# Optimization experiments

Hardware: AMD Instinct MI355X
Metric: run time of the kernel (lower is better)

## Reference

```python
import jax, jax.numpy as jnp
import numpy as np
from jax import lax

T, B, DIN, DLAT = 512, 512, 64, 128


def setup_inputs() -> dict:
    key = jax.random.key(0)
    ks = jax.random.split(key, 8)
    s = 0.1  # keep gate pre-activations in a sane range
    return {
        "seqs": jax.random.normal(ks[0], (T, B, DIN), dtype=jnp.float32),
        "h": jax.random.normal(ks[1], (B, DLAT), dtype=jnp.float32),
        "Wz": jax.random.normal(ks[2], (DLAT, DIN + DLAT), dtype=jnp.float32) * s,
        "bz": jax.random.normal(ks[3], (DLAT,), dtype=jnp.float32) * s,
        "Wr": jax.random.normal(ks[4], (DLAT, DIN + DLAT), dtype=jnp.float32) * s,
        "br": jax.random.normal(ks[5], (DLAT,), dtype=jnp.float32) * s,
        "Wi": jax.random.normal(ks[6], (DLAT, DIN + DLAT), dtype=jnp.float32) * s,
        "bi": jax.random.normal(ks[7], (DLAT,), dtype=jnp.float32) * s,
    }


def reference(seqs, h, Wz, bz, Wr, br, Wi, bi):
    # seqs: [T, B, DIN], h: [B, DLAT]. Returns all hiddens [T+1, B, DLAT].
    def step(h, x):
        merge = jnp.concatenate([h, x], axis=1)          # [B, DLAT+DIN]
        zt = jax.nn.sigmoid(merge @ Wz.T + bz)           # update gate
        rt = jax.nn.sigmoid(merge @ Wr.T + br)           # reset gate
        cand = jnp.tanh(jnp.concatenate([h * rt, x], axis=1) @ Wi.T + bi)
        h_new = (1.0 - zt) * h + zt * cand
        return h_new, h_new

    _, hs = lax.scan(step, h, seqs)                      # hs: [T, B, DLAT]
    return jnp.concatenate([h[None], hs], axis=0)        # [T+1, B, DLAT]
```

## Files before the change

### kernel.cpp

```cpp
#include <hip/hip_runtime.h>
#include <math.h>

#define TT   512
#define BB   512
#define DIN  64
#define DLAT 128
#define KKK  192
#define NBLK 32
#define TCHUNK 16
#define X_ELEMS ((size_t)TT * BB * 384)
#define X_BYTES (X_ELEMS * 2)

typedef _Float16 half8 __attribute__((ext_vector_type(8)));
typedef _Float16 half4 __attribute__((ext_vector_type(4)));
typedef float    f32x4 __attribute__((ext_vector_type(4)));

#define MFMA16(A, B, C) __builtin_amdgcn_mfma_f32_16x16x32_f16((A), (B), (C), 0, 0, 0)

__device__ __forceinline__ float fsigmoid(float x) {
    float e = __builtin_amdgcn_exp2f(-1.44269504f * x);
    return __builtin_amdgcn_rcpf(1.f + e);
}
__device__ __forceinline__ float ftanh(float x) {
    float e = __builtin_amdgcn_exp2f(2.88539008f * x);
    return 1.f - 2.f * __builtin_amdgcn_rcpf(1.f + e);
}
__device__ __forceinline__ half8 cvt8(float4 a, float4 b) {
    return (half8){(_Float16)a.x, (_Float16)a.y, (_Float16)a.z, (_Float16)a.w,
                   (_Float16)b.x, (_Float16)b.y, (_Float16)b.z, (_Float16)b.w};
}

__global__ __launch_bounds__(256) void xproj(
    const float* __restrict__ seqs,
    const float* __restrict__ Wz, const float* __restrict__ bz,
    const float* __restrict__ Wr, const float* __restrict__ br,
    const float* __restrict__ Wi, const float* __restrict__ bi,
    _Float16* __restrict__ X)
{
    const int tid = threadIdx.x;
    const int w = tid >> 6, l = tid & 63, q = l >> 4, ln = l & 15;
    const int bid = blockIdx.x;
    const int tb  = bid >> 5;
    const int blk = bid & 31;
    const int b0  = blk * 16;

    half8 wzf[2][2], wrf[2][2], wif[2][2];
    float bzv[2], brv[2], biv[2];
    #pragma unroll
    for (int s = 0; s < 2; ++s) {
        const int n = 32 * w + 16 * s + ln;
        #pragma unroll
        for (int kt = 0; kt < 2; ++kt) {
            const int k0 = DLAT + kt * 32 + q * 8;
            wzf[s][kt] = cvt8(*(const float4*)&Wz[n * KKK + k0],
                              *(const float4*)&Wz[n * KKK + k0 + 4]);
            wrf[s][kt] = cvt8(*(const float4*)&Wr[n * KKK + k0],
                              *(const float4*)&Wr[n * KKK + k0 + 4]);
            wif[s][kt] = cvt8(*(const float4*)&Wi[n * KKK + k0],
                              *(const float4*)&Wi[n * KKK + k0 + 4]);
        }
        bzv[s] = bz[n]; brv[s] = br[n]; biv[s] = bi[n];
    }

    for (int tt = 0; tt < TCHUNK; ++tt) {
        const int t = tb * TCHUNK + tt;
        const float* xr = seqs + ((size_t)t * BB + b0 + ln) * DIN + q * 8;
        half8 a0 = cvt8(*(const float4*)xr,        *(const float4*)(xr + 4));
        half8 a1 = cvt8(*(const float4*)(xr + 32), *(const float4*)(xr + 36));

        f32x4 az[2], ar[2], ai[2];
        #pragma unroll
        for (int s = 0; s < 2; ++s) {
            az[s] = (f32x4){bzv[s], bzv[s], bzv[s], bzv[s]};
            ar[s] = (f32x4){brv[s], brv[s], brv[s], brv[s]};
            ai[s] = (f32x4){biv[s], biv[s], biv[s], biv[s]};
        }
        #pragma unroll
        for (int s = 0; s < 2; ++s) {
            az[s] = MFMA16(a0, wzf[s][0], az[s]);
            az[s] = MFMA16(a1, wzf[s][1], az[s]);
            ar[s] = MFMA16(a0, wrf[s][0], ar[s]);
            ar[s] = MFMA16(a1, wrf[s][1], ar[s]);
            ai[s] = MFMA16(a0, wif[s][0], ai[s]);
            ai[s] = MFMA16(a1, wif[s][1], ai[s]);
        }

        half8 o0, o1, o2;
        #pragma unroll
        for (int s = 0; s < 2; ++s)
            #pragma unroll
            for (int i = 0; i < 4; ++i) {
                o0[s * 4 + i] = (_Float16)az[s][i];
                o1[s * 4 + i] = (_Float16)ar[s][i];
                o2[s * 4 + i] = (_Float16)ai[s][i];
            }
        _Float16* xo = X + ((size_t)(t * NBLK + blk) * 256 + tid) * 24;
        *(half8*)xo        = o0;
        *(half8*)(xo +  8) = o1;
        *(half8*)(xo + 16) = o2;
    }
}

__global__ __launch_bounds__(256, 1) void gru_rx(
    const float* __restrict__ h0,
    const float* __restrict__ Wz, const float* __restrict__ Wr,
    const float* __restrict__ Wi,
    const _Float16* __restrict__ X, float* __restrict__ out)
{
    __shared__ __align__(16) _Float16 hA [16][136];
    __shared__ __align__(16) _Float16 hrA[16][136];

    const int tid = threadIdx.x;
    const int w = tid >> 6, l = tid & 63, q = l >> 4, ln = l & 15;
    const int blk = (int)blockIdx.x;
    const int b0  = blk * 16;

    half8 wzf[2][4], wrf[2][4], wif[2][4];
    #pragma unroll
    for (int s = 0; s < 2; ++s) {
        const int n = 32 * w + 16 * s + ln;
        #pragma unroll
        for (int kt = 0; kt < 4; ++kt) {
            const int k0 = kt * 32 + q * 8;
            wzf[s][kt] = cvt8(*(const float4*)&Wz[n * KKK + k0],
                              *(const float4*)&Wz[n * KKK + k0 + 4]);
            wrf[s][kt] = cvt8(*(const float4*)&Wr[n * KKK + k0],
                              *(const float4*)&Wr[n * KKK + k0 + 4]);
            wif[s][kt] = cvt8(*(const float4*)&Wi[n * KKK + k0],
                              *(const float4*)&Wi[n * KKK + k0 + 4]);
        }
    }

    float h[2][4];
    #pragma unroll
    for (int s = 0; s < 2; ++s)
        #pragma unroll
        for (int i = 0; i < 4; ++i)
            h[s][i] = h0[(size_t)(b0 + 4 * q + i) * DLAT + 32 * w + 16 * s + ln];

    for (int idx = tid; idx < 16 * DLAT; idx += 256) {
        const int m = idx >> 7, c = idx & 127;
        const float v = h0[(size_t)(b0 + m) * DLAT + c];
        out[(size_t)(b0 + m) * DLAT + c] = v;
        hA[m][c] = (_Float16)v;
    }

    half8 xc0, xc1, xc2;
    {
        const _Float16* xp = X + ((size_t)(0 * NBLK + blk) * 256 + tid) * 24;
        xc0 = *(const half8*)xp;
        xc1 = *(const half8*)(xp + 8);
        xc2 = *(const half8*)(xp + 16);
    }
    __syncthreads();

    for (int t = 0; t < TT; ++t) {
        half8 xn0, xn1, xn2;
        const bool have = (t + 1 < TT);
        if (have) {
            const _Float16* xp = X + ((size_t)((t + 1) * NBLK + blk) * 256 + tid) * 24;
            xn0 = *(const half8*)xp;
            xn1 = *(const half8*)(xp + 8);
            xn2 = *(const half8*)(xp + 16);
        }

        half8 a0 = *(const half8*)&hA[ln][ 0 + q * 8];
        half8 a1 = *(const half8*)&hA[ln][32 + q * 8];
        half8 a2 = *(const half8*)&hA[ln][64 + q * 8];
        half8 a3 = *(const half8*)&hA[ln][96 + q * 8];

        f32x4 ar[2], az[2], ai[2];
        #pragma unroll
        for (int s = 0; s < 2; ++s)
            #pragma unroll
            for (int i = 0; i < 4; ++i) {
                ar[s][i] = (float)xc1[s * 4 + i];
                az[s][i] = (float)xc0[s * 4 + i];
            }
        #pragma unroll
        for (int s = 0; s < 2; ++s) {
            ar[s] = MFMA16(a0, wrf[s][0], ar[s]);
            ar[s] = MFMA16(a1, wrf[s][1], ar[s]);
            ar[s] = MFMA16(a2, wrf[s][2], ar[s]);
            ar[s] = MFMA16(a3, wrf[s][3], ar[s]);
        }
        #pragma unroll
        for (int s = 0; s < 2; ++s) {
            az[s] = MFMA16(a0, wzf[s][0], az[s]);
            az[s] = MFMA16(a1, wzf[s][1], az[s]);
            az[s] = MFMA16(a2, wzf[s][2], az[s]);
            az[s] = MFMA16(a3, wzf[s][3], az[s]);
        }
        #pragma unroll
        for (int s = 0; s < 2; ++s)
            #pragma unroll
            for (int i = 0; i < 4; ++i) {
                const float r = fsigmoid(ar[s][i]);
                hrA[4 * q + i][32 * w + 16 * s + ln] = (_Float16)(h[s][i] * r);
            }

        __syncthreads();

        half8 c0 = *(const half8*)&hrA[ln][ 0 + q * 8];
        half8 c1 = *(const half8*)&hrA[ln][32 + q * 8];
        half8 c2 = *(const half8*)&hrA[ln][64 + q * 8];
        half8 c3 = *(const half8*)&hrA[ln][96 + q * 8];
        #pragma unroll
        for (int s = 0; s < 2; ++s)
            #pragma unroll
            for (int i = 0; i < 4; ++i)
                ai[s][i] = (float)xc2[s * 4 + i];
        #pragma unroll
        for (int s = 0; s < 2; ++s) {
            ai[s] = MFMA16(c0, wif[s][0], ai[s]);
            ai[s] = MFMA16(c1, wif[s][1], ai[s]);
            ai[s] = MFMA16(c2, wif[s][2], ai[s]);
            ai[s] = MFMA16(c3, wif[s][3], ai[s]);
        }
        float zz[2][4];
        #pragma unroll
        for (int s = 0; s < 2; ++s)
            #pragma unroll
            for (int i = 0; i < 4; ++i)
                zz[s][i] = fsigmoid(az[s][i]);

        #pragma unroll
        for (int s = 0; s < 2; ++s)
            #pragma unroll
            for (int i = 0; i < 4; ++i) {
                const float cand = ftanh(ai[s][i]);
                const float hn   = h[s][i] + zz[s][i] * (cand - h[s][i]);
                h[s][i] = hn;
                const int m = 4 * q + i, c = 32 * w + 16 * s + ln;
                hA[m][c] = (_Float16)hn;
                out[((size_t)(t + 1) * BB + b0 + m) * DLAT + c] = hn;
            }

        xc0 = xn0; xc1 = xn1; xc2 = xn2;
        __syncthreads();
    }
}

__global__ __launch_bounds__(256, 1) void gru_mfma(
    const float* __restrict__ seqs, const float* __restrict__ h0,
    const float* __restrict__ bz, const float* __restrict__ br,
    const float* __restrict__ bi,
    const float* __restrict__ Wz, const float* __restrict__ Wr,
    const float* __restrict__ Wi, float* __restrict__ out)
{
    __shared__ __align__(16) _Float16 hA [16][136];
    __shared__ __align__(16) _Float16 hrA[16][136];
    __shared__ __align__(16) _Float16 xb [2][16][72];

    const int tid = threadIdx.x;
    const int w   = tid >> 6;
    const int l   = tid & 63;
    const int q   = l >> 4;
    const int ln  = l & 15;
    const int b0  = (int)blockIdx.x * 16;

    half8 wz[2][6], wr[2][6], wi[2][6];
    #pragma unroll
    for (int s = 0; s < 2; ++s) {
        const int n = 32 * w + 16 * s + ln;
        #pragma unroll
        for (int kt = 0; kt < 6; ++kt) {
            const int k0 = kt * 32 + q * 8;
            wz[s][kt] = cvt8(*(const float4*)&Wz[n * KKK + k0],
                             *(const float4*)&Wz[n * KKK + k0 + 4]);
            wr[s][kt] = cvt8(*(const float4*)&Wr[n * KKK + k0],
                             *(const float4*)&Wr[n * KKK + k0 + 4]);
            wi[s][kt] = cvt8(*(const float4*)&Wi[n * KKK + k0],
                             *(const float4*)&Wi[n * KKK + k0 + 4]);
        }
    }
    float bzv[2], brv[2], biv[2];
    #pragma unroll
    for (int s = 0; s < 2; ++s) {
        const int n = 32 * w + 16 * s + ln;
        bzv[s] = bz[n]; brv[s] = br[n]; biv[s] = bi[n];
    }

    float h[2][4];
    #pragma unroll
    for (int s = 0; s < 2; ++s)
        #pragma unroll
        for (int i = 0; i < 4; ++i)
            h[s][i] = h0[(size_t)(b0 + 4 * q + i) * DLAT + 32 * w + 16 * s + ln];

    for (int idx = tid; idx < 16 * DLAT; idx += 256) {
        const int m = idx >> 7, c = idx & 127;
        const float v = h0[(size_t)(b0 + m) * DLAT + c];
        out[(size_t)(b0 + m) * DLAT + c] = v;
        hA[m][c] = (_Float16)v;
    }
    {
        const int m = tid >> 4, k4 = tid & 15;
        const float4 xv = *(const float4*)&seqs[((size_t)0 * BB + b0 + m) * DIN + k4 * 4];
        *(half4*)&xb[0][m][k4 * 4] =
            (half4){(_Float16)xv.x, (_Float16)xv.y, (_Float16)xv.z, (_Float16)xv.w};
    }
    __syncthreads();

    for (int t = 0; t < TT; ++t) {
        const int p = t & 1;
        float4 xv;
        const int xm = tid >> 4, xk = tid & 15;
        if (t + 1 < TT)
            xv = *(const float4*)&seqs[((size_t)(t + 1) * BB + b0 + xm) * DIN + xk * 4];

        half8 a0 = *(const half8*)&hA[ln][ 0 + q * 8];
        half8 a1 = *(const half8*)&hA[ln][32 + q * 8];
        half8 a2 = *(const half8*)&hA[ln][64 + q * 8];
        half8 a3 = *(const half8*)&hA[ln][96 + q * 8];
        half8 x0 = *(const half8*)&xb[p][ln][ 0 + q * 8];
        half8 x1 = *(const half8*)&xb[p][ln][32 + q * 8];

        f32x4 az[2], ar[2], ai[2];
        #pragma unroll
        for (int s = 0; s < 2; ++s) {
            az[s] = (f32x4){bzv[s], bzv[s], bzv[s], bzv[s]};
            ar[s] = (f32x4){brv[s], brv[s], brv[s], brv[s]};
            ai[s] = (f32x4){biv[s], biv[s], biv[s], biv[s]};
        }
        #pragma unroll
        for (int s = 0; s < 2; ++s) {
            az[s] = MFMA16(x0, wz[s][4], az[s]);
            az[s] = MFMA16(x1, wz[s][5], az[s]);
            ar[s] = MFMA16(x0, wr[s][4], ar[s]);
            ar[s] = MFMA16(x1, wr[s][5], ar[s]);
            ai[s] = MFMA16(x0, wi[s][4], ai[s]);
            ai[s] = MFMA16(x1, wi[s][5], ai[s]);
            az[s] = MFMA16(a0, wz[s][0], az[s]);
            az[s] = MFMA16(a1, wz[s][1], az[s]);
            az[s] = MFMA16(a2, wz[s][2], az[s]);
            az[s] = MFMA16(a3, wz[s][3], az[s]);
            ar[s] = MFMA16(a0, wr[s][0], ar[s]);
            ar[s] = MFMA16(a1, wr[s][1], ar[s]);
            ar[s] = MFMA16(a2, wr[s][2], ar[s]);
            ar[s] = MFMA16(a3, wr[s][3], ar[s]);
        }

        float zz[2][4];
        #pragma unroll
        for (int s = 0; s < 2; ++s)
            #pragma unroll
            for (int i = 0; i < 4; ++i) {
                zz[s][i]      = fsigmoid(az[s][i]);
                const float r = fsigmoid(ar[s][i]);
                hrA[4 * q + i][32 * w + 16 * s + ln] = (_Float16)(h[s][i] * r);
            }

        if (t + 1 < TT)
            *(half4*)&xb[p ^ 1][xm][xk * 4] =
                (half4){(_Float16)xv.x, (_Float16)xv.y, (_Float16)xv.z, (_Float16)xv.w};

        __syncthreads();

        half8 c0 = *(const half8*)&hrA[ln][ 0 + q * 8];
        half8 c1 = *(const half8*)&hrA[ln][32 + q * 8];
        half8 c2 = *(const half8*)&hrA[ln][64 + q * 8];
        half8 c3 = *(const half8*)&hrA[ln][96 + q * 8];
        #pragma unroll
        for (int s = 0; s < 2; ++s) {
            ai[s] = MFMA16(c0, wi[s][0], ai[s]);
            ai[s] = MFMA16(c1, wi[s][1], ai[s]);
            ai[s] = MFMA16(c2, wi[s][2], ai[s]);
            ai[s] = MFMA16(c3, wi[s][3], ai[s]);
        }

        #pragma unroll
        for (int s = 0; s < 2; ++s)
            #pragma unroll
            for (int i = 0; i < 4; ++i) {
                const float cand = ftanh(ai[s][i]);
                const float hn   = h[s][i] + zz[s][i] * (cand - h[s][i]);
                h[s][i] = hn;
                const int m = 4 * q + i, c = 32 * w + 16 * s + ln;
                hA[m][c] = (_Float16)hn;
                out[((size_t)(t + 1) * BB + b0 + m) * DLAT + c] = hn;
            }

        __syncthreads();
    }
}

extern "C" void kernel_launch(void* const* d_in, const int* in_sizes, int n_in,
                              void* d_out, int out_size, void* d_ws, size_t ws_size,
                              hipStream_t stream) {
    const float* seqs = (const float*)d_in[0];
    const float* h0   = (const float*)d_in[1];
    const float* Wz   = (const float*)d_in[2];
    const float* bz   = (const float*)d_in[3];
    const float* Wr   = (const float*)d_in[4];
    const float* br   = (const float*)d_in[5];
    const float* Wi   = (const float*)d_in[6];
    const float* bi   = (const float*)d_in[7];
    float* out = (float*)d_out;

    if (ws_size >= X_BYTES) {
        _Float16* X = (_Float16*)d_ws;
        xproj<<<(TT / TCHUNK) * NBLK, 256, 0, stream>>>(seqs, Wz, bz, Wr, br, Wi, bi, X);
        gru_rx<<<NBLK, 256, 0, stream>>>(h0, Wz, Wr, Wi, X, out);
    } else {
        gru_mfma<<<NBLK, 256, 0, stream>>>(seqs, h0, bz, br, bi, Wz, Wr, Wi, out);
    }
}
```

Before: 591.7 us.

## Split recurrent GRU block across eight waves, one column tile each

The recurrent kernel now runs 512 threads per block instead of 256, so each of the eight waves owns a single 16-column output tile rather than two. This halves the serial MFMA chain and the gate math per wave on every time step, cutting latency on the critical path of the recurrence. Precomputed input projections are now loaded as half4 slices that match the new wave-to-column mapping. In exchange, the per-step barriers must synchronise twice as many waves and per-wave register use changes.

```diff
diff --git a/kernel.cpp b/kernel.cpp
--- a/kernel.cpp
+++ b/kernel.cpp
@@ -101,7 +101,7 @@
     }
 }
 
-__global__ __launch_bounds__(256, 1) void gru_rx(
+__global__ __launch_bounds__(512, 2) void gru_rx(
     const float* __restrict__ h0,
     const float* __restrict__ Wz, const float* __restrict__ Wr,
     const float* __restrict__ Wi,
@@ -111,57 +111,57 @@
     __shared__ __align__(16) _Float16 hrA[16][136];
 
     const int tid = threadIdx.x;
-    const int w = tid >> 6, l = tid & 63, q = l >> 4, ln = l & 15;
+    const int w   = tid >> 6;
+    const int l   = tid & 63;
+    const int q   = l >> 4;
+    const int ln  = l & 15;
     const int blk = (int)blockIdx.x;
     const int b0  = blk * 16;
-
-    half8 wzf[2][4], wrf[2][4], wif[2][4];
-    #pragma unroll
-    for (int s = 0; s < 2; ++s) {
-        const int n = 32 * w + 16 * s + ln;
-        #pragma unroll
-        for (int kt = 0; kt < 4; ++kt) {
-            const int k0 = kt * 32 + q * 8;
-            wzf[s][kt] = cvt8(*(const float4*)&Wz[n * KKK + k0],
-                              *(const float4*)&Wz[n * KKK + k0 + 4]);
-            wrf[s][kt] = cvt8(*(const float4*)&Wr[n * KKK + k0],
-                              *(const float4*)&Wr[n * KKK + k0 + 4]);
-            wif[s][kt] = cvt8(*(const float4*)&Wi[n * KKK + k0],
-                              *(const float4*)&Wi[n * KKK + k0 + 4]);
-        }
-    }
-
-    float h[2][4];
-    #pragma unroll
-    for (int s = 0; s < 2; ++s)
-        #pragma unroll
-        for (int i = 0; i < 4; ++i)
-            h[s][i] = h0[(size_t)(b0 + 4 * q + i) * DLAT + 32 * w + 16 * s + ln];
-
-    for (int idx = tid; idx < 16 * DLAT; idx += 256) {
+    const int nc  = 16 * w + ln;
+
+    half8 wzf[4], wrf[4], wif[4];
+    #pragma unroll
+    for (int kt = 0; kt < 4; ++kt) {
+        const int k0 = kt * 32 + q * 8;
+        wzf[kt] = cvt8(*(const float4*)&Wz[nc * KKK + k0],
+                       *(const float4*)&Wz[nc * KKK + k0 + 4]);
+        wrf[kt] = cvt8(*(const float4*)&Wr[nc * KKK + k0],
+                       *(const float4*)&Wr[nc * KKK + k0 + 4]);
+        wif[kt] = cvt8(*(const float4*)&Wi[nc * KKK + k0],
+                       *(const float4*)&Wi[nc * KKK + k0 + 4]);
+    }
+
+    float h[4];
+    #pragma unroll
+    for (int i = 0; i < 4; ++i)
+        h[i] = h0[(size_t)(b0 + 4 * q + i) * DLAT + nc];
+
+    for (int idx = tid; idx < 16 * DLAT; idx += 512) {
         const int m = idx >> 7, c = idx & 127;
         const float v = h0[(size_t)(b0 + m) * DLAT + c];
         out[(size_t)(b0 + m) * DLAT + c] = v;
         hA[m][c] = (_Float16)v;
     }
 
-    half8 xc0, xc1, xc2;
+    const size_t xslot = (size_t)((w >> 1) * 64 + q * 16 + ln) * 24 + (w & 1) * 4;
+
+    half4 xc0, xc1, xc2;
     {
-        const _Float16* xp = X + ((size_t)(0 * NBLK + blk) * 256 + tid) * 24;
-        xc0 = *(const half8*)xp;
-        xc1 = *(const half8*)(xp + 8);
-        xc2 = *(const half8*)(xp + 16);
+        const _Float16* xp = X + ((size_t)(0 * NBLK + blk) * 256) * 24 + xslot;
+        xc0 = *(const half4*)xp;
+        xc1 = *(const half4*)(xp + 8);
+        xc2 = *(const half4*)(xp + 16);
     }
     __syncthreads();
 
     for (int t = 0; t < TT; ++t) {
-        half8 xn0, xn1, xn2;
+        half4 xn0, xn1, xn2;
         const bool have = (t + 1 < TT);
         if (have) {
-            const _Float16* xp = X + ((size_t)((t + 1) * NBLK + blk) * 256 + tid) * 24;
-            xn0 = *(const half8*)xp;
-            xn1 = *(const half8*)(xp + 8);
-            xn2 = *(const half8*)(xp + 16);
+            const _Float16* xp = X + ((size_t)((t + 1) * NBLK + blk) * 256) * 24 + xslot;
+            xn0 = *(const half4*)xp;
+            xn1 = *(const half4*)(xp + 8);
+            xn2 = *(const half4*)(xp + 16);
         }
 
         half8 a0 = *(const half8*)&hA[ln][ 0 + q * 8];
@@ -169,35 +169,25 @@
         half8 a2 = *(const half8*)&hA[ln][64 + q * 8];
         half8 a3 = *(const half8*)&hA[ln][96 + q * 8];
 
-        f32x4 ar[2], az[2], ai[2];
-        #pragma unroll
-        for (int s = 0; s < 2; ++s)
-            #pragma unroll
-            for (int i = 0; i < 4; ++i) {
-                ar[s][i] = (float)xc1[s * 4 + i];
-                az[s][i] = (float)xc0[s * 4 + i];
-            }
-        #pragma unroll
-        for (int s = 0; s < 2; ++s) {
-            ar[s] = MFMA16(a0, wrf[s][0], ar[s]);
-            ar[s] = MFMA16(a1, wrf[s][1], ar[s]);
-            ar[s] = MFMA16(a2, wrf[s][2], ar[s]);
-            ar[s] = MFMA16(a3, wrf[s][3], ar[s]);
-        }
-        #pragma unroll
-        for (int s = 0; s < 2; ++s) {
-            az[s] = MFMA16(a0, wzf[s][0], az[s]);
-            az[s] = MFMA16(a1, wzf[s][1], az[s]);
-            az[s] = MFMA16(a2, wzf[s][2], az[s]);
-            az[s] = MFMA16(a3, wzf[s][3], az[s]);
-        }
-        #pragma unroll
-        for (int s = 0; s < 2; ++s)
-            #pragma unroll
-            for (int i = 0; i < 4; ++i) {
-                const float r = fsigmoid(ar[s][i]);
-                hrA[4 * q + i][32 * w + 16 * s + ln] = (_Float16)(h[s][i] * r);
-            }
+        f32x4 ar, az, ai;
+        #pragma unroll
+        for (int i = 0; i < 4; ++i) {
+            ar[i] = (float)xc1[i];
+            az[i] = (float)xc0[i];
+        }
+        ar = MFMA16(a0, wrf[0], ar);
+        ar = MFMA16(a1, wrf[1], ar);
+        ar = MFMA16(a2, wrf[2], ar);
+        ar = MFMA16(a3, wrf[3], ar);
+        az = MFMA16(a0, wzf[0], az);
+        az = MFMA16(a1, wzf[1], az);
+        az = MFMA16(a2, wzf[2], az);
+        az = MFMA16(a3, wzf[3], az);
+        #pragma unroll
+        for (int i = 0; i < 4; ++i) {
+            const float r = fsigmoid(ar[i]);
+            hrA[4 * q + i][nc] = (_Float16)(h[i] * r);
+        }
 
         __syncthreads();
 
@@ -206,35 +196,26 @@
         half8 c2 = *(const half8*)&hrA[ln][64 + q * 8];
         half8 c3 = *(const half8*)&hrA[ln][96 + q * 8];
         #pragma unroll
-        for (int s = 0; s < 2; ++s)
-            #pragma unroll
-            for (int i = 0; i < 4; ++i)
-                ai[s][i] = (float)xc2[s * 4 + i];
-        #pragma unroll
-        for (int s = 0; s < 2; ++s) {
-            ai[s] = MFMA16(c0, wif[s][0], ai[s]);
-            ai[s] = MFMA16(c1, wif[s][1], ai[s]);
-            ai[s] = MFMA16(c2, wif[s][2], ai[s]);
-            ai[s] = MFMA16(c3, wif[s][3], ai[s]);
-        }
-        float zz[2][4];
-        #pragma unroll
-        for (int s = 0; s < 2; ++s)
-            #pragma unroll
-            for (int i = 0; i < 4; ++i)
-                zz[s][i] = fsigmoid(az[s][i]);
-
-        #pragma unroll
-        for (int s = 0; s < 2; ++s)
-            #pragma unroll
-            for (int i = 0; i < 4; ++i) {
-                const float cand = ftanh(ai[s][i]);
-                const float hn   = h[s][i] + zz[s][i] * (cand - h[s][i]);
-                h[s][i] = hn;
-                const int m = 4 * q + i, c = 32 * w + 16 * s + ln;
-                hA[m][c] = (_Float16)hn;
-                out[((size_t)(t + 1) * BB + b0 + m) * DLAT + c] = hn;
-            }
+        for (int i = 0; i < 4; ++i)
+            ai[i] = (float)xc2[i];
+        ai = MFMA16(c0, wif[0], ai);
+        ai = MFMA16(c1, wif[1], ai);
+        ai = MFMA16(c2, wif[2], ai);
+        ai = MFMA16(c3, wif[3], ai);
+
+        float zz[4];
+        #pragma unroll
+        for (int i = 0; i < 4; ++i)
+            zz[i] = fsigmoid(az[i]);
+
+        #pragma unroll
+        for (int i = 0; i < 4; ++i) {
+            const float cand = ftanh(ai[i]);
+            const float hn   = h[i] + zz[i] * (cand - h[i]);
+            h[i] = hn;
+            hA[4 * q + i][nc] = (_Float16)hn;
+            out[((size_t)(t + 1) * BB + b0 + 4 * q + i) * DLAT + nc] = hn;
+        }
 
         xc0 = xn0; xc1 = xn1; xc2 = xn2;
         __syncthreads();
@@ -401,7 +382,7 @@
     if (ws_size >= X_BYTES) {
         _Float16* X = (_Float16*)d_ws;
         xproj<<<(TT / TCHUNK) * NBLK, 256, 0, stream>>>(seqs, Wz, bz, Wr, br, Wi, bi, X);
-        gru_rx<<<NBLK, 256, 0, stream>>>(h0, Wz, Wr, Wi, X, out);
+        gru_rx<<<NBLK, 512, 0, stream>>>(h0, Wz, Wr, Wi, X, out);
     } else {
         gru_mfma<<<NBLK, 256, 0, stream>>>(seqs, h0, bz, br, bi, Wz, Wr, Wi, out);
     }
```

After: 508.6 us. -14.0%, faster.
